# Performance work log

Measured on AMD Instinct MI355X. Metric: run time of the kernel, lower is better.

## Reference

```python
import jax, jax.numpy as jnp
import numpy as np

B, D, F = 2048, 512, 16384
K = 3
AUX_THR = 0.7
EPS = 1e-8


def setup_inputs() -> dict:
    key = jax.random.key(0)
    ks = jax.random.split(key, 14)
    sc_e = 1.0 / np.sqrt(D)
    sc_d = 1.0 / np.sqrt(F)
    return {
        "model_activations": jax.random.normal(ks[0], (B, D), jnp.float32),
        "We": jax.random.normal(ks[1], (F, D), jnp.float32) * sc_e,
        "be": jax.random.normal(ks[2], (F,), jnp.float32) * 0.01,
        "Wd": jax.random.normal(ks[3], (D, F), jnp.float32) * sc_d,
        "bd": jax.random.normal(ks[4], (D,), jnp.float32) * 0.01,
        "We1": jax.random.normal(ks[5], (F, D), jnp.float32) * sc_e,
        "be1": jax.random.normal(ks[6], (F,), jnp.float32) * 0.01,
        "Wd1": jax.random.normal(ks[7], (D, F), jnp.float32) * sc_d,
        "bd1": jax.random.normal(ks[8], (D,), jnp.float32) * 0.01,
        "We2": jax.random.normal(ks[9], (F, D), jnp.float32) * sc_e,
        "be2": jax.random.normal(ks[10], (F,), jnp.float32) * 0.01,
        "Wd2": jax.random.normal(ks[11], (D, F), jnp.float32) * sc_d,
        "bd2": jax.random.normal(ks[12], (D,), jnp.float32) * 0.01,
    }


def _forward(x, We, be, Wd, bd, We1, be1, Wd1, bd1, We2, be2, Wd2, bd2):
    # parent encoder + top-k scatter
    pre = x @ We.T + be                                   # [B, F]
    vals, idx = jax.lax.top_k(pre, K)                     # [B, K]
    sae = jnp.zeros_like(pre).at[jnp.arange(B)[:, None], idx].set(vals)

    # child routing
    pre1 = x @ We1.T + be1
    pre2 = x @ We2.T + be2
    sae_nz = sae != 0.0
    m1 = jnp.where(sae_nz, pre1, 0.0)
    m2 = jnp.where(sae_nz, pre2, 0.0)
    winners = m1 > m2
    fa1 = jnp.where(winners, m1, 0.0)
    fa2 = jnp.where(~winners, m2, 0.0)

    recon = (sae @ Wd.T + bd) + (fa1 @ Wd1.T + bd1) + (fa2 @ Wd2.T + bd2)

    # live-latent counts (as arrays, jit-friendly)
    n_parent = jnp.zeros((F,), jnp.float32).at[idx.reshape(-1)].set(1.0).sum().astype(jnp.int32)
    n_c1 = jnp.any(fa1 != 0, axis=0).sum().astype(jnp.int32)
    n_c2 = jnp.any(fa2 != 0, axis=0).sum().astype(jnp.int32)

    # auxiliary cosine loss, computed per-feature without materializing
    # the [B, D, F] scaled_parent / combined_weights tensors:
    #   scaled_parent[b,:,f] = a * Wd[:,f],  scaled_child[b,:,f] = c * Wc[:,f]
    # cos over D reduces to per-feature Gram terms.
    pp = jnp.sum(Wd * Wd, axis=0)      # [F] ||Wp_f||^2
    p1 = jnp.sum(Wd * Wd1, axis=0)     # [F] Wp_f . W1_f
    p2 = jnp.sum(Wd * Wd2, axis=0)
    s11 = jnp.sum(Wd1 * Wd1, axis=0)
    s22 = jnp.sum(Wd2 * Wd2, axis=0)

    a = sae                                              # [B, F]
    c = jnp.where(winners, fa1, fa2)                     # [B, F]
    pc = jnp.where(winners, p1[None, :], p2[None, :])    # [B, F]
    cc = jnp.where(winners, s11[None, :], s22[None, :])

    dot = a * (a * pp[None, :] + c * pc)                 # <scaled_parent, combined>
    nx = jnp.abs(a) * jnp.sqrt(pp)[None, :]              # ||scaled_parent||
    ny2 = a * a * pp[None, :] + 2.0 * a * c * pc + c * c * cc
    ny = jnp.sqrt(jnp.maximum(ny2, 0.0))                 # ||combined||
    cos = dot / (jnp.maximum(nx, EPS) * jnp.maximum(ny, EPS))

    active = (a > 0).astype(cos.dtype)
    sim_loss = jnp.maximum(0.0, AUX_THR - cos) * active
    aux = sim_loss.sum() / (active.sum() + 1e-08)

    return recon, (n_parent, n_c1, n_c2), aux


def reference(model_activations, We, be, Wd, bd, We1, be1, Wd1, bd1, We2, be2, Wd2, bd2):
    return _forward(model_activations, We, be, Wd, bd, We1, be1, Wd1, bd1, We2, be2, Wd2, bd2)
```

## Files before the change

kernel.cpp:

```cpp
#include <hip/hip_runtime.h>
#include <math.h>

#define B_DIM 2048
#define D_DIM 512
#define F_DIM 16384
#define K_TOP 3

typedef __attribute__((ext_vector_type(8))) short bf16x8;
typedef __attribute__((ext_vector_type(4))) float f32x4;

#define GL16(gsrc, ldst) \
  __builtin_amdgcn_global_load_lds( \
      (__attribute__((address_space(1))) const void*)(gsrc), \
      (__attribute__((address_space(3))) void*)(ldst), 16, 0, 0)

#define WAITVMCNT(n) asm volatile("s_waitcnt vmcnt(" #n ")" ::: "memory")
#define BARRIER() do { asm volatile("" ::: "memory"); \
    __builtin_amdgcn_s_barrier(); \
    asm volatile("" ::: "memory"); } while (0)

__device__ __forceinline__ bool better(float v, int c, float w, int j) {
    return (v > w) || (v == w && c < j);
}

__device__ __forceinline__ void ins3(float v, int c,
    float& v0, int& i0, float& v1, int& i1, float& v2, int& i2)
{
    if (!better(v, c, v2, i2)) return;
    if (better(v, c, v1, i1)) {
        v2 = v1; i2 = i1;
        if (better(v, c, v0, i0)) { v1 = v0; i1 = i0; v0 = v; i0 = c; }
        else { v1 = v; i1 = c; }
    } else { v2 = v; i2 = c; }
}

__device__ __forceinline__ uint okey(uint b16, int col) {
    uint m = 0x8000u + ((b16 >> 15) * 0x7FFFu);
    return ((b16 ^ m) << 14) | (uint)(16383 - col);
}

__device__ __forceinline__ void insK8(uint k, uint* V) {
#pragma unroll
    for (int j = 0; j < 8; ++j) {
        uint hi = V[j] > k ? V[j] : k;
        uint lo = V[j] > k ? k : V[j];
        V[j] = hi; k = lo;
    }
}

__device__ __forceinline__ void insK3(uint k, uint& V0, uint& V1, uint& V2) {
    uint h0 = V0 > k ? V0 : k, l0 = V0 > k ? k : V0; V0 = h0; k = l0;
    uint h1 = V1 > k ? V1 : k, l1 = V1 > k ? k : V1; V1 = h1; k = l1;
    V2 = V2 > k ? V2 : k;
}

__device__ __forceinline__ float bf2f(ushort u) {
    return __uint_as_float((uint)u << 16);
}

__device__ __forceinline__ uint pk(uint lo, uint hi) {
    return (hi & 0xFFFF0000u) | (lo >> 16);
}

__device__ __forceinline__ ushort bf_t(float v) {
    return (ushort)(__float_as_uint(v) >> 16);
}

__global__ __launch_bounds__(512) void prep_kernel(
    const float* __restrict__ Wd, const float* __restrict__ Wd1,
    const float* __restrict__ Wd2, ushort* __restrict__ WdT,
    ushort* __restrict__ Wd1T, ushort* __restrict__ Wd2T,
    float* __restrict__ gramp, int* __restrict__ flags3F,
    const float* __restrict__ We, ushort* __restrict__ We_bf,
    const float* __restrict__ x, ushort* __restrict__ x_bf)
{
    const int bid = blockIdx.x;
    const int t = threadIdx.x;

    if (bid >= 512) {
        const float* src; ushort* dst; int i;
        if (bid < 1536) { src = We; dst = We_bf; i = (bid - 512) * 1024 + t * 2; }
        else            { src = x;  dst = x_bf;  i = (bid - 1536) * 1024 + t * 2; }
#pragma unroll
        for (int u = 0; u < 2; ++u) {
            float4 a = ((const float4*)src)[(i + u) * 2];
            float4 b = ((const float4*)src)[(i + u) * 2 + 1];
            uint4 o;
            o.x = pk(__float_as_uint(a.x), __float_as_uint(a.y));
            o.y = pk(__float_as_uint(a.z), __float_as_uint(a.w));
            o.z = pk(__float_as_uint(b.x), __float_as_uint(b.y));
            o.w = pk(__float_as_uint(b.z), __float_as_uint(b.w));
            ((uint4*)dst)[i + u] = o;
        }
        return;
    }

    if (t < 24)
        ((uint4*)flags3F)[bid * 24 + t] = make_uint4(0, 0, 0, 0);

    __shared__ float tA[64][65], tB[64][65], tC[64][65];
    const int f0 = (bid >> 1) << 6;
    const int half = bid & 1;
    const int dl = t >> 3;
    const int fq = t & 7;
    const int flw = t >> 3;
    const int dg = t & 7;
    float pp = 0, p1 = 0, p2 = 0, s11 = 0, s22 = 0;

    float4 a0, a1, b0, b1, c0, c1;
#define LOADCH(chg) do { \
    const size_t base = (size_t)((chg) * 64 + dl) * F_DIM + f0 + fq * 8; \
    a0 = *(const float4*)(Wd  + base); a1 = *(const float4*)(Wd  + base + 4); \
    b0 = *(const float4*)(Wd1 + base); b1 = *(const float4*)(Wd1 + base + 4); \
    c0 = *(const float4*)(Wd2 + base); c1 = *(const float4*)(Wd2 + base + 4); \
} while (0)

    LOADCH(half * 4);
#pragma unroll 1
    for (int ch = 0; ch < 4; ++ch) {
        const int chg = half * 4 + ch;
        if (ch) __syncthreads();
        tA[dl][fq * 8 + 0] = a0.x; tA[dl][fq * 8 + 1] = a0.y;
        tA[dl][fq * 8 + 2] = a0.z; tA[dl][fq * 8 + 3] = a0.w;
        tA[dl][fq * 8 + 4] = a1.x; tA[dl][fq * 8 + 5] = a1.y;
        tA[dl][fq * 8 + 6] = a1.z; tA[dl][fq * 8 + 7] = a1.w;
        tB[dl][fq * 8 + 0] = b0.x; tB[dl][fq * 8 + 1] = b0.y;
        tB[dl][fq * 8 + 2] = b0.z; tB[dl][fq * 8 + 3] = b0.w;
        tB[dl][fq * 8 + 4] = b1.x; tB[dl][fq * 8 + 5] = b1.y;
        tB[dl][fq * 8 + 6] = b1.z; tB[dl][fq * 8 + 7] = b1.w;
        tC[dl][fq * 8 + 0] = c0.x; tC[dl][fq * 8 + 1] = c0.y;
        tC[dl][fq * 8 + 2] = c0.z; tC[dl][fq * 8 + 3] = c0.w;
        tC[dl][fq * 8 + 4] = c1.x; tC[dl][fq * 8 + 5] = c1.y;
        tC[dl][fq * 8 + 6] = c1.z; tC[dl][fq * 8 + 7] = c1.w;
        if (ch < 3) LOADCH(chg + 1);
        __syncthreads();
        ushort ua[8], ub[8], uc[8];
#pragma unroll
        for (int j = 0; j < 8; ++j) {
            float va = tA[dg * 8 + j][flw];
            float vb = tB[dg * 8 + j][flw];
            float vc = tC[dg * 8 + j][flw];
            pp  = fmaf(va, va, pp);
            p1  = fmaf(va, vb, p1);
            p2  = fmaf(va, vc, p2);
            s11 = fmaf(vb, vb, s11);
            s22 = fmaf(vc, vc, s22);
            ua[j] = bf_t(va); ub[j] = bf_t(vb); uc[j] = bf_t(vc);
        }
        const size_t doff = (size_t)(f0 + flw) * D_DIM + chg * 64 + dg * 8;
        *(uint4*)&WdT[doff] = make_uint4(
            ua[0] | ((uint)ua[1] << 16), ua[2] | ((uint)ua[3] << 16),
            ua[4] | ((uint)ua[5] << 16), ua[6] | ((uint)ua[7] << 16));
        *(uint4*)&Wd1T[doff] = make_uint4(
            ub[0] | ((uint)ub[1] << 16), ub[2] | ((uint)ub[3] << 16),
            ub[4] | ((uint)ub[5] << 16), ub[6] | ((uint)ub[7] << 16));
        *(uint4*)&Wd2T[doff] = make_uint4(
            uc[0] | ((uint)uc[1] << 16), uc[2] | ((uint)uc[3] << 16),
            uc[4] | ((uint)uc[5] << 16), uc[6] | ((uint)uc[7] << 16));
    }
#undef LOADCH

#pragma unroll
    for (int mk = 1; mk <= 4; mk <<= 1) {
        pp  += __shfl_xor(pp, mk);
        p1  += __shfl_xor(p1, mk);
        p2  += __shfl_xor(p2, mk);
        s11 += __shfl_xor(s11, mk);
        s22 += __shfl_xor(s22, mk);
    }
    if ((t & 7) == 0) {
        float* gp = gramp + (size_t)half * 5 * F_DIM;
        const int fcol = f0 + (t >> 3);
        gp[fcol] = pp;
        gp[F_DIM + fcol] = p1;
        gp[2 * F_DIM + fcol] = p2;
        gp[3 * F_DIM + fcol] = s11;
        gp[4 * F_DIM + fcol] = s22;
    }
}

__global__ __launch_bounds__(256) void gemm_kernel(
    const ushort* __restrict__ xb, const ushort* __restrict__ web,
    const float* __restrict__ be, uint* __restrict__ packed)
{
    __shared__ __align__(16) ushort As[2][4096];
    __shared__ __align__(16) ushort Bs[2][4096];

    const int t = threadIdx.x;
    const int id = blockIdx.x;
    const int r = id & 127;
    const int bx = ((r & 7) << 4) + (r >> 3);
    const int by = id >> 7;
    const int l = t & 63;
    const int w = t >> 6;
    const int wr = w >> 1, wc = w & 1;
    const int bm0 = by << 7;
    const int fn0 = bx << 7;
    const int frow = l & 15;
    const int q = l >> 4;

    const int srow = t >> 2;
    const int sgr = (t & 3) ^ ((t >> 3) & 3);
    const int soff = sgr << 3;
    const ushort* gA0 = xb + (size_t)(bm0 + srow) * D_DIM + soff;
    const ushort* gA1 = xb + (size_t)(bm0 + 64 + srow) * D_DIM + soff;
    const ushort* gB0 = web + (size_t)(fn0 + srow) * D_DIM + soff;
    const ushort* gB1 = web + (size_t)(fn0 + 64 + srow) * D_DIM + soff;

#define STAGE(bufp, koff) do { \
    GL16(gA0 + (koff), (char*)As + (bufp) * 8192 + t * 16); \
    GL16(gA1 + (koff), (char*)As + (bufp) * 8192 + 4096 + t * 16); \
    GL16(gB0 + (koff), (char*)Bs + (bufp) * 8192 + t * 16); \
    GL16(gB1 + (koff), (char*)Bs + (bufp) * 8192 + 4096 + t * 16); \
} while (0)

    f32x4 acc[4][4];
#pragma unroll
    for (int m = 0; m < 4; ++m)
#pragma unroll
        for (int n = 0; n < 4; ++n) acc[m][n] = (f32x4)(0.f);

    const int qs = (q ^ ((frow >> 1) & 3)) << 3;
    const int aoff = (wr * 64 + frow) * 32 + qs;
    const int boff = (wc * 64 + frow) * 32 + qs;

    STAGE(0, 0);

#pragma unroll 1
    for (int t16 = 0; t16 < 16; ++t16) {
        const int cur = t16 & 1;
        if (t16 < 15) {
            STAGE(cur ^ 1, (t16 + 1) * 32);
            WAITVMCNT(4);
        } else {
            WAITVMCNT(0);
        }
        BARRIER();
        const ushort* Ab = &As[0][0] + cur * 4096 + aoff;
        const ushort* Bb = &Bs[0][0] + cur * 4096 + boff;
        bf16x8 af[4], bfr[4];
#pragma unroll
        for (int m = 0; m < 4; ++m) af[m] = *(const bf16x8*)(Ab + m * 512);
#pragma unroll
        for (int n = 0; n < 4; ++n) bfr[n] = *(const bf16x8*)(Bb + n * 512);
#pragma unroll
        for (int m = 0; m < 4; ++m)
#pragma unroll
            for (int n = 0; n < 4; ++n)
                acc[m][n] = __builtin_amdgcn_mfma_f32_16x16x32_bf16(
                    af[m], bfr[n], acc[m][n], 0, 0, 0);
        BARRIER();
    }
#undef STAGE

    float bias[4];
#pragma unroll
    for (int n = 0; n < 4; ++n) bias[n] = be[fn0 + wc * 64 + n * 16 + frow];

    const int colb = fn0 + wc * 64 + frow;
    const int rowbase = bm0 + wr * 64 + (q << 2);
    const int tile2 = (bx << 1) + wc;
#pragma unroll
    for (int m = 0; m < 4; ++m) {
#pragma unroll
        for (int i = 0; i < 4; ++i) {
            uint V0 = 0, V1 = 0, V2 = 0;
#pragma unroll
            for (int n = 0; n < 4; ++n) {
                float v = acc[m][n][i] + bias[n];
                uint key = okey(__float_as_uint(v) >> 16, colb + n * 16);
                insK3(key, V0, V1, V2);
            }
#pragma unroll
            for (int mk = 1; mk <= 8; mk <<= 1) {
                uint o0 = (uint)__shfl_xor((int)V0, mk);
                uint o1 = (uint)__shfl_xor((int)V1, mk);
                uint o2 = (uint)__shfl_xor((int)V2, mk);
                insK3(o0, V0, V1, V2);
                insK3(o1, V0, V1, V2);
                insK3(o2, V0, V1, V2);
            }
            if (frow == 0) {
                uint* dp = packed + (size_t)(rowbase + m * 16 + i) * 768 + tile2 * 3;
                dp[0] = V0; dp[1] = V1; dp[2] = V2;
            }
        }
    }
}

__global__ __launch_bounds__(512) void mrcra_kernel(
    const uint* __restrict__ packed,
    const float* __restrict__ x, const float* __restrict__ We,
    const float* __restrict__ be,
    const float* __restrict__ We1, const float* __restrict__ be1,
    const float* __restrict__ We2, const float* __restrict__ be2,
    const float* __restrict__ gramp,
    const ushort* __restrict__ WdT, const float* __restrict__ bd,
    const ushort* __restrict__ Wd1T, const float* __restrict__ bd1,
    const ushort* __restrict__ Wd2T, const float* __restrict__ bd2,
    int* __restrict__ flagP, int* __restrict__ flag1, int* __restrict__ flag2,
    float* __restrict__ auxpart, float* __restrict__ cntpart,
    float* __restrict__ out)
{
    __shared__ int sc8[8];
    __shared__ float sv[8];
    __shared__ int si[8];
    __shared__ float sval[3], sdot[3][2], scv[3], sterm[3], sact[3];
    __shared__ int sidx[3], swin[3];
    const int row = blockIdx.x;
    const int t = threadIdx.x;
    const int wv = t >> 6, l = t & 63;

    if (t < 64) {
        const uint* p = packed + (size_t)row * 768;
        uint V[8] = {0, 0, 0, 0, 0, 0, 0, 0};
#pragma unroll
        for (int m = 0; m < 12; ++m) {
            uint k = p[t + (m << 6)];
            if (k > V[7]) insK8(k, V);
        }
#pragma unroll
        for (int mk = 1; mk < 64; mk <<= 1) {
            uint o[8];
#pragma unroll
            for (int j = 0; j < 8; ++j) o[j] = (uint)__shfl_xor((int)V[j], mk);
#pragma unroll
            for (int j = 0; j < 8; ++j)
                if (o[j] > V[7]) insK8(o[j], V);
        }
        if (t == 0) {
#pragma unroll
            for (int j = 0; j < 8; ++j)
                sc8[j] = 16383 - (int)(V[j] & 16383u);
        }
    }
    __syncthreads();

    {
        const int f = sc8[wv];
        const float* xr = x + (size_t)row * D_DIM;
        const float* wp = We + (size_t)f * D_DIM;
        float s = 0.f;
#pragma unroll
        for (int m = 0; m < 8; ++m) { int e = l + (m << 6); s = fmaf(xr[e], wp[e], s); }
#pragma unroll
        for (int mk = 1; mk < 64; mk <<= 1) s += __shfl_xor(s, mk);
        if (l == 0) { sv[wv] = s + be[f]; si[wv] = f; }
    }
    __syncthreads();
    if (t == 0) {
        float v0 = -INFINITY, v1 = -INFINITY, v2 = -INFINITY;
        int i0 = 0x7fffffff, i1 = 0x7fffffff, i2 = 0x7fffffff;
        for (int k = 0; k < 8; ++k) ins3(sv[k], si[k], v0, i0, v1, i1, v2, i2);
        sval[0] = v0; sidx[0] = i0;
        sval[1] = v1; sidx[1] = i1;
        sval[2] = v2; sidx[2] = i2;
    }
    __syncthreads();

    if (wv < 6) {
        const int p = wv >> 1, mt = wv & 1;
        const int f = sidx[p];
        const float* wp = (mt ? We2 : We1) + (size_t)f * D_DIM;
        const float* xr = x + (size_t)row * D_DIM;
        float s = 0.f;
#pragma unroll
        for (int m = 0; m < 8; ++m) { int e = l + (m << 6); s = fmaf(xr[e], wp[e], s); }
#pragma unroll
        for (int mk = 1; mk < 64; mk <<= 1) s += __shfl_xor(s, mk);
        if (l == 0) sdot[p][mt] = s + (mt ? be2 : be1)[f];
    }
    __syncthreads();

    if (t < 3) {
        const int p = t;
        const float a = sval[p];
        const int f = sidx[p];
        float m1 = (a != 0.f) ? sdot[p][0] : 0.f;
        float m2 = (a != 0.f) ? sdot[p][1] : 0.f;
        bool win = m1 > m2;
        float fa1 = win ? m1 : 0.f;
        float fa2 = win ? 0.f : m2;
        float cv = win ? fa1 : fa2;
        scv[p] = cv; swin[p] = win ? 1 : 0;
        flagP[f] = 1;
        if (fa1 != 0.f) flag1[f] = 1;
        if (fa2 != 0.f) flag2[f] = 1;
        const int gsel = win ? 1 : 2;
        const int ssel = win ? 3 : 4;
        const float pp = gramp[f] + gramp[5 * F_DIM + f];
        const float pc = gramp[gsel * F_DIM + f] + gramp[(5 + gsel) * F_DIM + f];
        const float cc = gramp[ssel * F_DIM + f] + gramp[(5 + ssel) * F_DIM + f];
        const float dot = a * (a * pp + cv * pc);
        const float nx = fabsf(a) * sqrtf(pp);
        const float ny2 = a * a * pp + 2.f * a * cv * pc + cv * cv * cc;
        const float ny = sqrtf(fmaxf(ny2, 0.f));
        const float cosv = dot / (fmaxf(nx, 1e-8f) * fmaxf(ny, 1e-8f));
        sterm[p] = (a > 0.f) ? fmaxf(0.f, 0.7f - cosv) : 0.f;
        sact[p] = (a > 0.f) ? 1.f : 0.f;
    }
    __syncthreads();
    if (t == 0) {
        auxpart[row] = sterm[0] + sterm[1] + sterm[2];
        cntpart[row] = sact[0] + sact[1] + sact[2];
    }

    const int d = t;
    float o = bd[d] + bd1[d] + bd2[d];
#pragma unroll
    for (int k = 0; k < 3; ++k) {
        const int f = sidx[k];
        const float a = sval[k];
        const float c = scv[k];
        const int win = swin[k];
        const size_t off = (size_t)f * D_DIM + d;
        o = fmaf(a, bf2f(WdT[off]), o);
        if (c != 0.f) {
            const ushort* wt = win ? Wd1T : Wd2T;
            o = fmaf(c, bf2f(wt[off]), o);
        }
    }
    out[(size_t)row * D_DIM + d] = o;
}

__global__ __launch_bounds__(256) void finalize_kernel(
    const int* __restrict__ flagP, const int* __restrict__ flag1,
    const int* __restrict__ flag2,
    const float* __restrict__ auxpart, const float* __restrict__ cntpart,
    float* __restrict__ out)
{
    const int t = threadIdx.x;
    int sp = 0, s1 = 0, s2 = 0;
    for (int f = t; f < F_DIM; f += 256) { sp += flagP[f]; s1 += flag1[f]; s2 += flag2[f]; }
    float asum = 0.f, acnt = 0.f;
    for (int i = t; i < B_DIM; i += 256) { asum += auxpart[i]; acnt += cntpart[i]; }
#pragma unroll
    for (int m = 1; m < 64; m <<= 1) {
        sp += __shfl_xor(sp, m); s1 += __shfl_xor(s1, m); s2 += __shfl_xor(s2, m);
        asum += __shfl_xor(asum, m); acnt += __shfl_xor(acnt, m);
    }
    __shared__ int red[3][4];
    __shared__ float fred[2][4];
    const int w = t >> 6;
    if ((t & 63) == 0) {
        red[0][w] = sp; red[1][w] = s1; red[2][w] = s2;
        fred[0][w] = asum; fred[1][w] = acnt;
    }
    __syncthreads();
    if (t == 0) {
        float np_ = (float)(red[0][0] + red[0][1] + red[0][2] + red[0][3]);
        float n1_ = (float)(red[1][0] + red[1][1] + red[1][2] + red[1][3]);
        float n2_ = (float)(red[2][0] + red[2][1] + red[2][2] + red[2][3]);
        float as = fred[0][0] + fred[0][1] + fred[0][2] + fred[0][3];
        float ac = fred[1][0] + fred[1][1] + fred[1][2] + fred[1][3];
        const size_t base = (size_t)B_DIM * D_DIM;
        out[base + 0] = np_;
        out[base + 1] = n1_;
        out[base + 2] = n2_;
        out[base + 3] = as / (ac + 1e-8f);
    }
}

extern "C" void kernel_launch(void* const* d_in, const int* in_sizes, int n_in,
                              void* d_out, int out_size, void* d_ws, size_t ws_size,
                              hipStream_t stream)
{
    (void)in_sizes; (void)n_in; (void)out_size; (void)ws_size;
    const float* x   = (const float*)d_in[0];
    const float* We  = (const float*)d_in[1];
    const float* be  = (const float*)d_in[2];
    const float* Wd  = (const float*)d_in[3];
    const float* bd  = (const float*)d_in[4];
    const float* We1 = (const float*)d_in[5];
    const float* be1 = (const float*)d_in[6];
    const float* Wd1 = (const float*)d_in[7];
    const float* bd1 = (const float*)d_in[8];
    const float* We2 = (const float*)d_in[9];
    const float* be2 = (const float*)d_in[10];
    const float* Wd2 = (const float*)d_in[11];
    const float* bd2 = (const float*)d_in[12];
    float* out = (float*)d_out;

    ushort* x_bf  = (ushort*)d_ws;
    ushort* We_bf = x_bf + (size_t)B_DIM * D_DIM;
    ushort* WdT   = We_bf + (size_t)F_DIM * D_DIM;
    ushort* Wd1T  = WdT + (size_t)F_DIM * D_DIM;
    ushort* Wd2T  = Wd1T + (size_t)F_DIM * D_DIM;
    uint*   packed = (uint*)(Wd2T + (size_t)F_DIM * D_DIM);
    float*  gramp = (float*)(packed + (size_t)B_DIM * 768);
    int*    flagP = (int*)(gramp + 10 * F_DIM);
    int*    flag1 = flagP + F_DIM;
    int*    flag2 = flag1 + F_DIM;
    float*  auxpart = (float*)(flag2 + F_DIM);
    float*  cntpart = auxpart + B_DIM;

    prep_kernel<<<1664, 512, 0, stream>>>(
        Wd, Wd1, Wd2, WdT, Wd1T, Wd2T, gramp, flagP,
        We, We_bf, x, x_bf);

    gemm_kernel<<<2048, 256, 0, stream>>>(x_bf, We_bf, be, packed);

    mrcra_kernel<<<B_DIM, 512, 0, stream>>>(
        packed, x, We, be, We1, be1, We2, be2, gramp,
        WdT, bd, Wd1T, bd1, Wd2T, bd2,
        flagP, flag1, flag2, auxpart, cntpart, out);

    finalize_kernel<<<1, 256, 0, stream>>>(
        flagP, flag1, flag2, auxpart, cntpart, out);
}
```

Before: 134.4 us.

## Move decoder-weight transpose and Gram sums into the GEMM launch

Splits the old prep kernel. The We/x bf16 conversion becomes a small standalone kernel, and the decoder-weight transpose, bf16 packing and per-feature Gram sums run as extra blocks appended to the encoder GEMM grid. The aim is to overlap the memory-bound transpose of the three decoder matrices with the compute-bound GEMM instead of running it before the GEMM. The transpose blocks are reshaped to 256 threads with 32-row chunks to share the GEMM's block size and shared-memory buffer. The risk is that they contend with GEMM blocks for bandwidth and CU slots, and the appended blocks may form a tail.

```diff
diff --git a/kernel.cpp b/kernel.cpp
--- a/kernel.cpp
+++ b/kernel.cpp
@@ -66,127 +66,116 @@
     return (ushort)(__float_as_uint(v) >> 16);
 }
 
-__global__ __launch_bounds__(512) void prep_kernel(
+__global__ __launch_bounds__(512) void convert_kernel(
+    const float* __restrict__ We, ushort* __restrict__ We_bf,
+    const float* __restrict__ x, ushort* __restrict__ x_bf)
+{
+    const float* src; ushort* dst; int i;
+    if (blockIdx.x < 1024) { src = We; dst = We_bf; i = blockIdx.x * 1024 + threadIdx.x * 2; }
+    else                   { src = x;  dst = x_bf;  i = (blockIdx.x - 1024) * 1024 + threadIdx.x * 2; }
+#pragma unroll
+    for (int u = 0; u < 2; ++u) {
+        float4 a = ((const float4*)src)[(i + u) * 2];
+        float4 b = ((const float4*)src)[(i + u) * 2 + 1];
+        uint4 o;
+        o.x = pk(__float_as_uint(a.x), __float_as_uint(a.y));
+        o.y = pk(__float_as_uint(a.z), __float_as_uint(a.w));
+        o.z = pk(__float_as_uint(b.x), __float_as_uint(b.y));
+        o.w = pk(__float_as_uint(b.z), __float_as_uint(b.w));
+        ((uint4*)dst)[i + u] = o;
+    }
+}
+
+__global__ __launch_bounds__(256) void gemmtr_kernel(
+    const ushort* __restrict__ xb, const ushort* __restrict__ web,
+    const float* __restrict__ be, uint* __restrict__ packed,
     const float* __restrict__ Wd, const float* __restrict__ Wd1,
     const float* __restrict__ Wd2, ushort* __restrict__ WdT,
     ushort* __restrict__ Wd1T, ushort* __restrict__ Wd2T,
-    float* __restrict__ gramp, int* __restrict__ flags3F,
-    const float* __restrict__ We, ushort* __restrict__ We_bf,
-    const float* __restrict__ x, ushort* __restrict__ x_bf)
-{
-    const int bid = blockIdx.x;
+    float* __restrict__ gramp, int* __restrict__ flags3F)
+{
+    __shared__ __align__(16) char smem[32768];
     const int t = threadIdx.x;
 
-    if (bid >= 512) {
-        const float* src; ushort* dst; int i;
-        if (bid < 1536) { src = We; dst = We_bf; i = (bid - 512) * 1024 + t * 2; }
-        else            { src = x;  dst = x_bf;  i = (bid - 1536) * 1024 + t * 2; }
-#pragma unroll
-        for (int u = 0; u < 2; ++u) {
-            float4 a = ((const float4*)src)[(i + u) * 2];
-            float4 b = ((const float4*)src)[(i + u) * 2 + 1];
-            uint4 o;
-            o.x = pk(__float_as_uint(a.x), __float_as_uint(a.y));
-            o.y = pk(__float_as_uint(a.z), __float_as_uint(a.w));
-            o.z = pk(__float_as_uint(b.x), __float_as_uint(b.y));
-            o.w = pk(__float_as_uint(b.z), __float_as_uint(b.w));
-            ((uint4*)dst)[i + u] = o;
+    if (blockIdx.x >= 2048) {
+        const int id2 = blockIdx.x - 2048;
+        if (t < 24)
+            ((uint4*)flags3F)[id2 * 24 + t] = make_uint4(0, 0, 0, 0);
+        float* tA = (float*)smem;
+        float* tB = tA + 32 * 65;
+        float* tC = tB + 32 * 65;
+        const int f0 = (id2 >> 1) << 6;
+        const int dbase = (id2 & 1) << 8;
+        const int dl = t >> 3, fq = t & 7;
+        const int flw = t >> 2, dg = t & 3;
+        float pp = 0, p1 = 0, p2 = 0, s11 = 0, s22 = 0;
+        float4 a0, a1, b0, b1, c0, c1;
+#define LOADCH(ch) do { \
+    const size_t base_ = (size_t)(dbase + (ch) * 32 + dl) * F_DIM + f0 + fq * 8; \
+    a0 = *(const float4*)(Wd  + base_); a1 = *(const float4*)(Wd  + base_ + 4); \
+    b0 = *(const float4*)(Wd1 + base_); b1 = *(const float4*)(Wd1 + base_ + 4); \
+    c0 = *(const float4*)(Wd2 + base_); c1 = *(const float4*)(Wd2 + base_ + 4); \
+} while (0)
+        LOADCH(0);
+#pragma unroll 1
+        for (int ch = 0; ch < 8; ++ch) {
+            if (ch) __syncthreads();
+            const int lb = dl * 65 + fq * 8;
+            tA[lb + 0] = a0.x; tA[lb + 1] = a0.y; tA[lb + 2] = a0.z; tA[lb + 3] = a0.w;
+            tA[lb + 4] = a1.x; tA[lb + 5] = a1.y; tA[lb + 6] = a1.z; tA[lb + 7] = a1.w;
+            tB[lb + 0] = b0.x; tB[lb + 1] = b0.y; tB[lb + 2] = b0.z; tB[lb + 3] = b0.w;
+            tB[lb + 4] = b1.x; tB[lb + 5] = b1.y; tB[lb + 6] = b1.z; tB[lb + 7] = b1.w;
+            tC[lb + 0] = c0.x; tC[lb + 1] = c0.y; tC[lb + 2] = c0.z; tC[lb + 3] = c0.w;
+            tC[lb + 4] = c1.x; tC[lb + 5] = c1.y; tC[lb + 6] = c1.z; tC[lb + 7] = c1.w;
+            if (ch < 7) LOADCH(ch + 1);
+            __syncthreads();
+            ushort ua[8], ub[8], uc[8];
+#pragma unroll
+            for (int j = 0; j < 8; ++j) {
+                float va = tA[(dg * 8 + j) * 65 + flw];
+                float vb = tB[(dg * 8 + j) * 65 + flw];
+                float vc = tC[(dg * 8 + j) * 65 + flw];
+                pp  = fmaf(va, va, pp);
+                p1  = fmaf(va, vb, p1);
+                p2  = fmaf(va, vc, p2);
+                s11 = fmaf(vb, vb, s11);
+                s22 = fmaf(vc, vc, s22);
+                ua[j] = bf_t(va); ub[j] = bf_t(vb); uc[j] = bf_t(vc);
+            }
+            const size_t doff = (size_t)(f0 + flw) * D_DIM + dbase + ch * 32 + dg * 8;
+            *(uint4*)&WdT[doff] = make_uint4(
+                ua[0] | ((uint)ua[1] << 16), ua[2] | ((uint)ua[3] << 16),
+                ua[4] | ((uint)ua[5] << 16), ua[6] | ((uint)ua[7] << 16));
+            *(uint4*)&Wd1T[doff] = make_uint4(
+                ub[0] | ((uint)ub[1] << 16), ub[2] | ((uint)ub[3] << 16),
+                ub[4] | ((uint)ub[5] << 16), ub[6] | ((uint)ub[7] << 16));
+            *(uint4*)&Wd2T[doff] = make_uint4(
+                uc[0] | ((uint)uc[1] << 16), uc[2] | ((uint)uc[3] << 16),
+                uc[4] | ((uint)uc[5] << 16), uc[6] | ((uint)uc[7] << 16));
+        }
+#undef LOADCH
+#pragma unroll
+        for (int mk = 1; mk <= 2; mk <<= 1) {
+            pp  += __shfl_xor(pp, mk);
+            p1  += __shfl_xor(p1, mk);
+            p2  += __shfl_xor(p2, mk);
+            s11 += __shfl_xor(s11, mk);
+            s22 += __shfl_xor(s22, mk);
+        }
+        if ((t & 3) == 0) {
+            float* gp = gramp + (size_t)(id2 & 1) * 5 * F_DIM;
+            const int fcol = f0 + (t >> 2);
+            gp[fcol] = pp;
+            gp[F_DIM + fcol] = p1;
+            gp[2 * F_DIM + fcol] = p2;
+            gp[3 * F_DIM + fcol] = s11;
+            gp[4 * F_DIM + fcol] = s22;
         }
         return;
     }
 
-    if (t < 24)
-        ((uint4*)flags3F)[bid * 24 + t] = make_uint4(0, 0, 0, 0);
-
-    __shared__ float tA[64][65], tB[64][65], tC[64][65];
-    const int f0 = (bid >> 1) << 6;
-    const int half = bid & 1;
-    const int dl = t >> 3;
-    const int fq = t & 7;
-    const int flw = t >> 3;
-    const int dg = t & 7;
-    float pp = 0, p1 = 0, p2 = 0, s11 = 0, s22 = 0;
-
-    float4 a0, a1, b0, b1, c0, c1;
-#define LOADCH(chg) do { \
-    const size_t base = (size_t)((chg) * 64 + dl) * F_DIM + f0 + fq * 8; \
-    a0 = *(const float4*)(Wd  + base); a1 = *(const float4*)(Wd  + base + 4); \
-    b0 = *(const float4*)(Wd1 + base); b1 = *(const float4*)(Wd1 + base + 4); \
-    c0 = *(const float4*)(Wd2 + base); c1 = *(const float4*)(Wd2 + base + 4); \
-} while (0)
-
-    LOADCH(half * 4);
-#pragma unroll 1
-    for (int ch = 0; ch < 4; ++ch) {
-        const int chg = half * 4 + ch;
-        if (ch) __syncthreads();
-        tA[dl][fq * 8 + 0] = a0.x; tA[dl][fq * 8 + 1] = a0.y;
-        tA[dl][fq * 8 + 2] = a0.z; tA[dl][fq * 8 + 3] = a0.w;
-        tA[dl][fq * 8 + 4] = a1.x; tA[dl][fq * 8 + 5] = a1.y;
-        tA[dl][fq * 8 + 6] = a1.z; tA[dl][fq * 8 + 7] = a1.w;
-        tB[dl][fq * 8 + 0] = b0.x; tB[dl][fq * 8 + 1] = b0.y;
-        tB[dl][fq * 8 + 2] = b0.z; tB[dl][fq * 8 + 3] = b0.w;
-        tB[dl][fq * 8 + 4] = b1.x; tB[dl][fq * 8 + 5] = b1.y;
-        tB[dl][fq * 8 + 6] = b1.z; tB[dl][fq * 8 + 7] = b1.w;
-        tC[dl][fq * 8 + 0] = c0.x; tC[dl][fq * 8 + 1] = c0.y;
-        tC[dl][fq * 8 + 2] = c0.z; tC[dl][fq * 8 + 3] = c0.w;
-        tC[dl][fq * 8 + 4] = c1.x; tC[dl][fq * 8 + 5] = c1.y;
-        tC[dl][fq * 8 + 6] = c1.z; tC[dl][fq * 8 + 7] = c1.w;
-        if (ch < 3) LOADCH(chg + 1);
-        __syncthreads();
-        ushort ua[8], ub[8], uc[8];
-#pragma unroll
-        for (int j = 0; j < 8; ++j) {
-            float va = tA[dg * 8 + j][flw];
-            float vb = tB[dg * 8 + j][flw];
-            float vc = tC[dg * 8 + j][flw];
-            pp  = fmaf(va, va, pp);
-            p1  = fmaf(va, vb, p1);
-            p2  = fmaf(va, vc, p2);
-            s11 = fmaf(vb, vb, s11);
-            s22 = fmaf(vc, vc, s22);
-            ua[j] = bf_t(va); ub[j] = bf_t(vb); uc[j] = bf_t(vc);
-        }
-        const size_t doff = (size_t)(f0 + flw) * D_DIM + chg * 64 + dg * 8;
-        *(uint4*)&WdT[doff] = make_uint4(
-            ua[0] | ((uint)ua[1] << 16), ua[2] | ((uint)ua[3] << 16),
-            ua[4] | ((uint)ua[5] << 16), ua[6] | ((uint)ua[7] << 16));
-        *(uint4*)&Wd1T[doff] = make_uint4(
-            ub[0] | ((uint)ub[1] << 16), ub[2] | ((uint)ub[3] << 16),
-            ub[4] | ((uint)ub[5] << 16), ub[6] | ((uint)ub[7] << 16));
-        *(uint4*)&Wd2T[doff] = make_uint4(
-            uc[0] | ((uint)uc[1] << 16), uc[2] | ((uint)uc[3] << 16),
-            uc[4] | ((uint)uc[5] << 16), uc[6] | ((uint)uc[7] << 16));
-    }
-#undef LOADCH
-
-#pragma unroll
-    for (int mk = 1; mk <= 4; mk <<= 1) {
-        pp  += __shfl_xor(pp, mk);
-        p1  += __shfl_xor(p1, mk);
-        p2  += __shfl_xor(p2, mk);
-        s11 += __shfl_xor(s11, mk);
-        s22 += __shfl_xor(s22, mk);
-    }
-    if ((t & 7) == 0) {
-        float* gp = gramp + (size_t)half * 5 * F_DIM;
-        const int fcol = f0 + (t >> 3);
-        gp[fcol] = pp;
-        gp[F_DIM + fcol] = p1;
-        gp[2 * F_DIM + fcol] = p2;
-        gp[3 * F_DIM + fcol] = s11;
-        gp[4 * F_DIM + fcol] = s22;
-    }
-}
-
-__global__ __launch_bounds__(256) void gemm_kernel(
-    const ushort* __restrict__ xb, const ushort* __restrict__ web,
-    const float* __restrict__ be, uint* __restrict__ packed)
-{
-    __shared__ __align__(16) ushort As[2][4096];
-    __shared__ __align__(16) ushort Bs[2][4096];
-
-    const int t = threadIdx.x;
+    ushort* As = (ushort*)smem;
+    ushort* Bs = As + 8192;
     const int id = blockIdx.x;
     const int r = id & 127;
     const int bx = ((r & 7) << 4) + (r >> 3);
@@ -236,8 +225,8 @@
             WAITVMCNT(0);
         }
         BARRIER();
-        const ushort* Ab = &As[0][0] + cur * 4096 + aoff;
-        const ushort* Bb = &Bs[0][0] + cur * 4096 + boff;
+        const ushort* Ab = As + cur * 4096 + aoff;
+        const ushort* Bb = Bs + cur * 4096 + boff;
         bf16x8 af[4], bfr[4];
 #pragma unroll
         for (int m = 0; m < 4; ++m) af[m] = *(const bf16x8*)(Ab + m * 512);
@@ -494,11 +483,11 @@
     float*  auxpart = (float*)(flag2 + F_DIM);
     float*  cntpart = auxpart + B_DIM;
 
-    prep_kernel<<<1664, 512, 0, stream>>>(
-        Wd, Wd1, Wd2, WdT, Wd1T, Wd2T, gramp, flagP,
-        We, We_bf, x, x_bf);
-
-    gemm_kernel<<<2048, 256, 0, stream>>>(x_bf, We_bf, be, packed);
+    convert_kernel<<<1152, 512, 0, stream>>>(We, We_bf, x, x_bf);
+
+    gemmtr_kernel<<<2560, 256, 0, stream>>>(
+        x_bf, We_bf, be, packed,
+        Wd, Wd1, Wd2, WdT, Wd1T, Wd2T, gramp, flagP);
 
     mrcra_kernel<<<B_DIM, 512, 0, stream>>>(
         packed, x, We, be, We1, be1, We2, be2, gramp,
```

Result: faster. 129.5 us, median of 2 (-3.6%).
